# Performance work log

Measured on AMD Instinct MI355X. Metric: run time of the kernel, lower is better.

The kernel has to match this reference:

```python
import jax, jax.numpy as jnp
import numpy as np

IN_F = 8192
OUT_F = 8192
R = 16
LORA_ALPHA = 32
BLOCK = 64
SCALING = LORA_ALPHA / R  # 2.0
NUMEL = IN_F * OUT_F


def dequantize_4bit(packed, scales):
    # packed: [numel//2] bytes (stored as int32 in [0,255]); element 2i = low nibble, 2i+1 = high nibble
    low = packed & 0xF
    high = (packed >> 4) & 0xF
    q = jnp.stack([low, high], axis=-1).reshape(-1)          # [numel] ints in [0,15]
    flat = q.astype(jnp.float32) - 8.0                        # signed 4-bit
    flat = (flat.reshape(-1, BLOCK) * scales[:, None]).reshape(-1)  # blockwise scale
    return flat.reshape(OUT_F, IN_F)


def setup_inputs() -> dict:
    key = jax.random.key(0)
    k1, k2, k3, k4, k5 = jax.random.split(key, 5)
    x = jax.random.normal(k1, (1, 64, IN_F), dtype=jnp.float32)
    packed_weights = jax.random.randint(k2, (NUMEL // 2,), 0, 256, dtype=jnp.int32)
    block_scales = jax.random.uniform(k3, (NUMEL // BLOCK,), dtype=jnp.float32) * 0.05
    # kaiming_uniform(a=sqrt(5)) on [R, IN_F] -> bound = 1/sqrt(IN_F)
    bound = 1.0 / np.sqrt(IN_F)
    lora_A = jax.random.uniform(k4, (R, IN_F), minval=-bound, maxval=bound, dtype=jnp.float32)
    # original init is zeros; use small randn for a non-trivial baseline
    lora_B = jax.random.normal(k5, (OUT_F, R), dtype=jnp.float32) * 0.02
    return {"x": x, "packed_weights": packed_weights, "block_scales": block_scales,
            "lora_A": lora_A, "lora_B": lora_B}


def reference(x, packed_weights, block_scales, lora_A, lora_B):
    W = dequantize_4bit(packed_weights, block_scales).astype(x.dtype)  # [OUT_F, IN_F]
    base_out = jnp.einsum('bsi,oi->bso', x, W)                         # no bias (bias_buffer=None)
    lora_out = jnp.einsum('bsr,or->bso', jnp.einsum('bsi,ri->bsr', x, lora_A), lora_B) * SCALING
    return base_out + lora_out
```

## Files before the change

### kernel.cpp

```cpp
#include <hip/hip_runtime.h>
#include <hip/hip_bf16.h>

#define IN_F 8192
#define OUT_F 8192
#define SEQ 64
#define LORA_R 16

typedef __attribute__((ext_vector_type(4))) float f32x4;
typedef __attribute__((ext_vector_type(4))) int i32x4;
typedef __attribute__((ext_vector_type(4))) unsigned short u16x4;
typedef _Float16 f16x2 __attribute__((ext_vector_type(2)));
typedef _Float16 f16x8 __attribute__((ext_vector_type(8)));

typedef __attribute__((address_space(3))) unsigned int lds_u32;
typedef const __attribute__((address_space(1))) unsigned int glb_u32;

__device__ __forceinline__ void gl_lds16(const void* g, void* l) {
    __builtin_amdgcn_global_load_lds((glb_u32*)g, (lds_u32*)l, 16, 0, 0);
}

#define VMCNT(n) asm volatile("s_waitcnt vmcnt(" #n ")" ::: "memory")

__global__ __launch_bounds__(256) void k_prep(
    const float* __restrict__ x, const float* __restrict__ A,
    unsigned short* __restrict__ xb, float* __restrict__ t) {
    __shared__ float part[64];
    const int s = blockIdx.x >> 2, p = blockIdx.x & 3;
    const int w = threadIdx.x >> 6, lane = threadIdx.x & 63;
    const int kbase = p * 2048 + w * 512;
    const float* xr = x + s * IN_F + kbase;

    f32x4 xv[2];
    #pragma unroll
    for (int j = 0; j < 2; ++j) {
        xv[j] = *(const f32x4*)(xr + j * 256 + lane * 4);
        u16x4 h;
        h[0] = __builtin_bit_cast(unsigned short, (_Float16)xv[j].x);
        h[1] = __builtin_bit_cast(unsigned short, (_Float16)xv[j].y);
        h[2] = __builtin_bit_cast(unsigned short, (_Float16)xv[j].z);
        h[3] = __builtin_bit_cast(unsigned short, (_Float16)xv[j].w);
        *(u16x4*)(xb + s * IN_F + kbase + j * 256 + lane * 4) = h;
    }

    float acc[LORA_R];
    #pragma unroll
    for (int r = 0; r < LORA_R; ++r) acc[r] = 0.f;
    #pragma unroll
    for (int r = 0; r < LORA_R; ++r) {
        const float* ar = A + r * IN_F + kbase;
        #pragma unroll
        for (int j = 0; j < 2; ++j) {
            f32x4 av = *(const f32x4*)(ar + j * 256 + lane * 4);
            acc[r] = fmaf(xv[j].x, av.x, acc[r]);
            acc[r] = fmaf(xv[j].y, av.y, acc[r]);
            acc[r] = fmaf(xv[j].z, av.z, acc[r]);
            acc[r] = fmaf(xv[j].w, av.w, acc[r]);
        }
    }
    #pragma unroll
    for (int r = 0; r < LORA_R; ++r) {
        float v = acc[r];
        #pragma unroll
        for (int off = 32; off; off >>= 1) v += __shfl_down(v, off, 64);
        if (lane == 0) part[w * 16 + r] = v;
    }
    __syncthreads();
    if (threadIdx.x < 16)
        t[s * 64 + p * 16 + threadIdx.x] = part[threadIdx.x] + part[16 + threadIdx.x] +
                                           part[32 + threadIdx.x] + part[48 + threadIdx.x];
}

__global__ __launch_bounds__(512, 2) void k_main(
    const int* __restrict__ packed, const float* __restrict__ scales,
    const unsigned short* __restrict__ xb, const float* __restrict__ t,
    const float* __restrict__ B, float* __restrict__ out) {
    __shared__ char lds[155904];
    _Float16* xs = (_Float16*)lds;
    int* wt = (int*)(lds + 98304);
    _Float16* scs = (_Float16*)(lds + 147456);
    float* accs = (float*)lds;
    float* tred = (float*)(lds + 36864);

    const int tid = threadIdx.x;
    const int n0 = blockIdx.x * 32;
    const int w = tid >> 6, lane = tid & 63;
    const int nh = w >> 2, wkk = w & 3;
    const int q = lane >> 4, c16 = lane & 15;
    const int l5 = lane >> 5, l31 = lane & 31;

    {
        int row = tid >> 4, g = tid & 15;
        const float* sp = scales + (n0 + row) * (IN_F / 64);
        f32x4 a = *(const f32x4*)(sp + g * 4);
        f32x4 b = *(const f32x4*)(sp + 64 + g * 4);
        u16x4 ha, hb;
        ha[0] = __builtin_bit_cast(unsigned short, (_Float16)a.x);
        ha[1] = __builtin_bit_cast(unsigned short, (_Float16)a.y);
        ha[2] = __builtin_bit_cast(unsigned short, (_Float16)a.z);
        ha[3] = __builtin_bit_cast(unsigned short, (_Float16)a.w);
        hb[0] = __builtin_bit_cast(unsigned short, (_Float16)b.x);
        hb[1] = __builtin_bit_cast(unsigned short, (_Float16)b.y);
        hb[2] = __builtin_bit_cast(unsigned short, (_Float16)b.z);
        hb[3] = __builtin_bit_cast(unsigned short, (_Float16)b.w);
        *(u16x4*)((unsigned short*)scs + row * 132 + g * 4) = ha;
        *(u16x4*)((unsigned short*)scs + row * 132 + 64 + g * 4) = hb;
    }

    const unsigned short* xg[4];
    #pragma unroll
    for (int j = 0; j < 4; ++j) {
        int row = 8 * w + 2 * j + l5;
        xg[j] = xb + (size_t)row * IN_F + ((l31 ^ (row & 7)) << 3);
    }
    _Float16* xd = xs + w * 2048;
    const int wr0 = 4 * w + l5, wr1 = wr0 + 2;
    const int* wg0 = packed + (size_t)(n0 + wr0) * (IN_F / 2) + ((l31 ^ (wr0 & 7)) << 2);
    const int* wg1 = packed + (size_t)(n0 + wr1) * (IN_F / 2) + ((l31 ^ (wr1 & 7)) << 2);
    int* wd = wt + w * 512;

    const int row_w = nh * 16 + c16, r7 = c16 & 7;
    const int pvo0 = row_w * 128 + ((4 * wkk + q) ^ r7) * 4;
    const int pvo1 = row_w * 128 + ((4 * (wkk + 4) + q) ^ r7) * 4;
    int afo0[4], afo1[4];
    #pragma unroll
    for (int mt = 0; mt < 4; ++mt) {
        afo0[mt] = (mt * 16 + c16) * 256 + ((4 * wkk + q) ^ r7) * 8;
        afo1[mt] = (mt * 16 + c16) * 256 + ((4 * (wkk + 4) + q) ^ r7) * 8;
    }
    const int scso = row_w * 132 + (wkk >> 1);

    f32x4 acc[4];
    #pragma unroll
    for (int mt = 0; mt < 4; ++mt) acc[mt] = (f32x4){0.f, 0.f, 0.f, 0.f};

    #pragma unroll
    for (int c = 0; c < 2; ++c) {
        #pragma unroll
        for (int j = 0; j < 4; ++j)
            gl_lds16(xg[j] + (size_t)c * 256, xd + c * 16384 + j * 512);
        gl_lds16(wg0 + (size_t)c * 128, wd + c * 4096);
        gl_lds16(wg1 + (size_t)c * 128, wd + c * 4096 + 256);
    }
    asm volatile("s_waitcnt lgkmcnt(0)" ::: "memory");
    __builtin_amdgcn_s_barrier();

    const f16x2 c1032 = {(_Float16)1032.0f, (_Float16)1032.0f};

    for (int kt = 0; kt < 32; ++kt) {
        if (kt < 31) VMCNT(6);
        else         VMCNT(0);
        __builtin_amdgcn_s_barrier();
        __builtin_amdgcn_sched_barrier(0);
        const int cb = kt % 3;
        if (kt <= 29) {
            const int nb = (kt + 2) % 3;
            const size_t xo = (size_t)(kt + 2) * 256;
            const size_t wo = (size_t)(kt + 2) * 128;
            #pragma unroll
            for (int j = 0; j < 4; ++j)
                gl_lds16(xg[j] + xo, xd + nb * 16384 + j * 512);
            gl_lds16(wg0 + wo, wd + nb * 4096);
            gl_lds16(wg1 + wo, wd + nb * 4096 + 256);
        }
        i32x4 pv0 = *(const i32x4*)(wt + cb * 4096 + pvo0);
        i32x4 pv1 = *(const i32x4*)(wt + cb * 4096 + pvo1);
        _Float16 s0 = scs[scso + kt * 4];
        _Float16 s1 = scs[scso + kt * 4 + 2];
        f16x2 sc0 = {s0, s0}, sc1 = {s1, s1};
        f16x8 bf0, bf1;
        #pragma unroll
        for (int m = 0; m < 4; ++m) {
            unsigned u0 = ((((unsigned)pv0[m] << 12) | (unsigned)pv0[m]) & 0x000F000Fu) | 0x64006400u;
            unsigned u1 = ((((unsigned)pv1[m] << 12) | (unsigned)pv1[m]) & 0x000F000Fu) | 0x64006400u;
            f16x2 h0 = __builtin_bit_cast(f16x2, u0);
            f16x2 h1 = __builtin_bit_cast(f16x2, u1);
            h0 = (h0 - c1032) * sc0;
            h1 = (h1 - c1032) * sc1;
            bf0[2 * m] = h0.x; bf0[2 * m + 1] = h0.y;
            bf1[2 * m] = h1.x; bf1[2 * m + 1] = h1.y;
        }
        const _Float16* xbase = xs + cb * 16384;
        #pragma unroll
        for (int mt = 0; mt < 4; ++mt) {
            f16x8 af = *(const f16x8*)(xbase + afo0[mt]);
            acc[mt] = __builtin_amdgcn_mfma_f32_16x16x32_f16(af, bf0, acc[mt], 0, 0, 0);
        }
        #pragma unroll
        for (int mt = 0; mt < 4; ++mt) {
            f16x8 af = *(const f16x8*)(xbase + afo1[mt]);
            acc[mt] = __builtin_amdgcn_mfma_f32_16x16x32_f16(af, bf1, acc[mt], 0, 0, 0);
        }
    }
    __syncthreads();

    float* myacc = accs + w * (64 * 17);
    #pragma unroll
    for (int mt = 0; mt < 4; ++mt)
        #pragma unroll
        for (int r = 0; r < 4; ++r)
            myacc[(mt * 16 + q * 4 + r) * 17 + c16] = acc[mt][r];
    #pragma unroll
    for (int jj = 0; jj < 2; ++jj) {
        int p2 = tid + jj * 512;
        const float* tp = t + (p2 >> 4) * 64 + (p2 & 15);
        tred[p2] = tp[0] + tp[16] + tp[32] + tp[48];
    }
    __syncthreads();

    #pragma unroll
    for (int j = 0; j < 4; ++j) {
        int p = tid + j * 512;
        int s = p >> 5, c = p & 31;
        const float* ab = accs + (c >> 4) * 4 * (64 * 17) + s * 17 + (c & 15);
        float v = ab[0] + ab[64 * 17] + ab[2 * 64 * 17] + ab[3 * 64 * 17];
        const float* trow = tred + s * 16;
        const float* bp = B + (n0 + c) * LORA_R;
        f32x4 t0 = *(const f32x4*)trow,        t1 = *(const f32x4*)(trow + 4);
        f32x4 t2 = *(const f32x4*)(trow + 8),  t3 = *(const f32x4*)(trow + 12);
        f32x4 b0 = *(const f32x4*)bp,       b1 = *(const f32x4*)(bp + 4);
        f32x4 b2 = *(const f32x4*)(bp + 8), b3 = *(const f32x4*)(bp + 12);
        float lr = t0.x * b0.x + t0.y * b0.y + t0.z * b0.z + t0.w * b0.w
                 + t1.x * b1.x + t1.y * b1.y + t1.z * b1.z + t1.w * b1.w
                 + t2.x * b2.x + t2.y * b2.y + t2.z * b2.z + t2.w * b2.w
                 + t3.x * b3.x + t3.y * b3.y + t3.z * b3.z + t3.w * b3.w;
        v += 2.0f * lr;
        out[s * OUT_F + n0 + c] = v;
    }
}

extern "C" void kernel_launch(void* const* d_in, const int* in_sizes, int n_in,
                              void* d_out, int out_size, void* d_ws, size_t ws_size,
                              hipStream_t stream) {
    const float* x      = (const float*)d_in[0];
    const int* packed   = (const int*)d_in[1];
    const float* scales = (const float*)d_in[2];
    const float* lora_A = (const float*)d_in[3];
    const float* lora_B = (const float*)d_in[4];
    float* out = (float*)d_out;

    unsigned short* xb = (unsigned short*)d_ws;
    float* t = (float*)((char*)d_ws + (size_t)SEQ * IN_F * 2);

    k_prep<<<256, 256, 0, stream>>>(x, lora_A, xb, t);
    k_main<<<256, 512, 0, stream>>>(packed, scales, xb, t, lora_B, out);
}
```

Measured before the change: 210.3 us.

## Load activations directly into registers and quad-buffer weight tiles in LDS

Activation tiles are no longer staged through LDS with global_load_lds. Each wave now loads its MFMA A fragments straight from global memory (expected to hit L2) into registers. The LDS footprint shrinks to just the packed weights and scales, and the freed space lets the weight pipeline grow from three to four buffers with a deeper prefetch distance. The explicit per-iteration vmcnt waits are dropped, so correctness now relies on compiler-inserted waits for the register loads. Activation loads are issued in the same iteration they are consumed, which risks exposed latency and duplicated L2 reads across waves.

```diff
diff --git a/kernel.cpp b/kernel.cpp
--- a/kernel.cpp
+++ b/kernel.cpp
@@ -74,10 +74,9 @@
     const int* __restrict__ packed, const float* __restrict__ scales,
     const unsigned short* __restrict__ xb, const float* __restrict__ t,
     const float* __restrict__ B, float* __restrict__ out) {
-    __shared__ char lds[155904];
-    _Float16* xs = (_Float16*)lds;
-    int* wt = (int*)(lds + 98304);
-    _Float16* scs = (_Float16*)(lds + 147456);
+    __shared__ char lds[73984];
+    int* wt = (int*)lds;
+    _Float16* scs = (_Float16*)(lds + 65536);
     float* accs = (float*)lds;
     float* tred = (float*)(lds + 36864);
 
@@ -105,28 +104,21 @@
         *(u16x4*)((unsigned short*)scs + row * 132 + g * 4) = ha;
         *(u16x4*)((unsigned short*)scs + row * 132 + 64 + g * 4) = hb;
     }
-
-    const unsigned short* xg[4];
-    #pragma unroll
-    for (int j = 0; j < 4; ++j) {
-        int row = 8 * w + 2 * j + l5;
-        xg[j] = xb + (size_t)row * IN_F + ((l31 ^ (row & 7)) << 3);
-    }
-    _Float16* xd = xs + w * 2048;
+    __builtin_amdgcn_sched_barrier(0);
+
     const int wr0 = 4 * w + l5, wr1 = wr0 + 2;
     const int* wg0 = packed + (size_t)(n0 + wr0) * (IN_F / 2) + ((l31 ^ (wr0 & 7)) << 2);
     const int* wg1 = packed + (size_t)(n0 + wr1) * (IN_F / 2) + ((l31 ^ (wr1 & 7)) << 2);
     int* wd = wt + w * 512;
 
+    const _Float16* xf[4];
+    #pragma unroll
+    for (int mt = 0; mt < 4; ++mt)
+        xf[mt] = (const _Float16*)xb + (size_t)(mt * 16 + c16) * IN_F + (4 * wkk + q) * 8;
+
     const int row_w = nh * 16 + c16, r7 = c16 & 7;
     const int pvo0 = row_w * 128 + ((4 * wkk + q) ^ r7) * 4;
     const int pvo1 = row_w * 128 + ((4 * (wkk + 4) + q) ^ r7) * 4;
-    int afo0[4], afo1[4];
-    #pragma unroll
-    for (int mt = 0; mt < 4; ++mt) {
-        afo0[mt] = (mt * 16 + c16) * 256 + ((4 * wkk + q) ^ r7) * 8;
-        afo1[mt] = (mt * 16 + c16) * 256 + ((4 * (wkk + 4) + q) ^ r7) * 8;
-    }
     const int scso = row_w * 132 + (wkk >> 1);
 
     f32x4 acc[4];
@@ -134,31 +126,29 @@
     for (int mt = 0; mt < 4; ++mt) acc[mt] = (f32x4){0.f, 0.f, 0.f, 0.f};
 
     #pragma unroll
-    for (int c = 0; c < 2; ++c) {
-        #pragma unroll
-        for (int j = 0; j < 4; ++j)
-            gl_lds16(xg[j] + (size_t)c * 256, xd + c * 16384 + j * 512);
+    for (int c = 0; c < 3; ++c) {
         gl_lds16(wg0 + (size_t)c * 128, wd + c * 4096);
         gl_lds16(wg1 + (size_t)c * 128, wd + c * 4096 + 256);
     }
+    VMCNT(4);
     asm volatile("s_waitcnt lgkmcnt(0)" ::: "memory");
     __builtin_amdgcn_s_barrier();
 
     const f16x2 c1032 = {(_Float16)1032.0f, (_Float16)1032.0f};
 
     for (int kt = 0; kt < 32; ++kt) {
-        if (kt < 31) VMCNT(6);
-        else         VMCNT(0);
         __builtin_amdgcn_s_barrier();
         __builtin_amdgcn_sched_barrier(0);
-        const int cb = kt % 3;
-        if (kt <= 29) {
-            const int nb = (kt + 2) % 3;
-            const size_t xo = (size_t)(kt + 2) * 256;
-            const size_t wo = (size_t)(kt + 2) * 128;
-            #pragma unroll
-            for (int j = 0; j < 4; ++j)
-                gl_lds16(xg[j] + xo, xd + nb * 16384 + j * 512);
+        const int cb = kt & 3;
+        f16x8 af0[4], af1[4];
+        #pragma unroll
+        for (int mt = 0; mt < 4; ++mt) {
+            af0[mt] = *(const f16x8*)(xf[mt] + kt * 256);
+            af1[mt] = *(const f16x8*)(xf[mt] + kt * 256 + 128);
+        }
+        if (kt <= 28) {
+            const size_t wo = (size_t)(kt + 3) * 128;
+            const int nb = (kt + 3) & 3;
             gl_lds16(wg0 + wo, wd + nb * 4096);
             gl_lds16(wg1 + wo, wd + nb * 4096 + 256);
         }
@@ -179,17 +169,12 @@
             bf0[2 * m] = h0.x; bf0[2 * m + 1] = h0.y;
             bf1[2 * m] = h1.x; bf1[2 * m + 1] = h1.y;
         }
-        const _Float16* xbase = xs + cb * 16384;
-        #pragma unroll
-        for (int mt = 0; mt < 4; ++mt) {
-            f16x8 af = *(const f16x8*)(xbase + afo0[mt]);
-            acc[mt] = __builtin_amdgcn_mfma_f32_16x16x32_f16(af, bf0, acc[mt], 0, 0, 0);
-        }
-        #pragma unroll
-        for (int mt = 0; mt < 4; ++mt) {
-            f16x8 af = *(const f16x8*)(xbase + afo1[mt]);
-            acc[mt] = __builtin_amdgcn_mfma_f32_16x16x32_f16(af, bf1, acc[mt], 0, 0, 0);
-        }
+        #pragma unroll
+        for (int mt = 0; mt < 4; ++mt)
+            acc[mt] = __builtin_amdgcn_mfma_f32_16x16x32_f16(af0[mt], bf0, acc[mt], 0, 0, 0);
+        #pragma unroll
+        for (int mt = 0; mt < 4; ++mt)
+            acc[mt] = __builtin_amdgcn_mfma_f32_16x16x32_f16(af1[mt], bf1, acc[mt], 0, 0, 0);
     }
     __syncthreads();
 
```

Result: slower. 249.0 us (+18.4%).
